# Optimization experiments

Hardware: AMD Instinct MI355X
Metric: run time of the kernel (lower is better)

The kernel has to match this reference:

```python
import jax, jax.numpy as jnp
import numpy as np

H = 12  # num_heads

def _alibi_bias(num_heads, n, dtype):
    # slopes: ratio**i for i in 1..H, ratio = 2**(-8/H)
    ratio = 2.0 ** (-8.0 / num_heads)
    slopes = ratio ** jnp.arange(1, num_heads + 1, dtype=jnp.float32)  # [H]
    pos = jnp.arange(n)
    rel = jnp.abs(pos[None, :] - pos[:, None]).astype(jnp.float32)  # [N,N]
    return (-slopes[:, None, None] * rel[None]).astype(dtype)  # [H,N,N]

def setup_inputs() -> dict:
    key = jax.random.key(0)
    ks = jax.random.split(key, 5)
    B, N, C = 16, 1024, 768
    s = 0.02
    return {
        "x": jax.random.normal(ks[0], (B, N, C), jnp.float32),
        "w_qkv": jax.random.normal(ks[1], (3 * C, C), jnp.float32) * s,
        "b_qkv": jax.random.normal(ks[2], (3 * C,), jnp.float32) * s,
        "w_proj": jax.random.normal(ks[3], (C, C), jnp.float32) * s,
        "b_proj": jax.random.normal(ks[4], (C,), jnp.float32) * s,
    }

def reference(x, w_qkv, b_qkv, w_proj, b_proj):
    B, N, C = x.shape
    D = C // H
    scale = D ** -0.5
    qkv = x @ w_qkv.T + b_qkv                       # [B,N,3C]
    qkv = qkv.reshape(B, N, 3, H, D)
    q = qkv[:, :, 0].transpose(0, 2, 1, 3)          # [B,H,N,D]
    k = qkv[:, :, 1].transpose(0, 2, 1, 3)
    v = qkv[:, :, 2].transpose(0, 2, 1, 3)
    bias = _alibi_bias(H, N, x.dtype)               # [H,N,N]
    scores = jnp.einsum('bhnd,bhmd->bhnm', q, k) * scale + bias[None]
    attn = jax.nn.softmax(scores, axis=-1)
    out = jnp.einsum('bhnm,bhmd->bhnd', attn, v)    # [B,H,N,D]
    out = out.transpose(0, 2, 1, 3).reshape(B, N, C)
    return out @ w_proj.T + b_proj
```

## Files before the change

kernel.cpp:

```cpp
#include <hip/hip_runtime.h>


typedef unsigned short u16;
typedef unsigned int u32;
typedef __attribute__((ext_vector_type(8))) short short8;
typedef __attribute__((ext_vector_type(4))) float f32x4;

__device__ __forceinline__ u16 f2bf(float f) {
    u32 u = __float_as_uint(f);
    u32 r = u + 0x7FFFu + ((u >> 16) & 1u);
    return (u16)(r >> 16);
}

__device__ __forceinline__ f32x4 mfma16(short8 a, short8 b, f32x4 c) {
    return __builtin_amdgcn_mfma_f32_16x16x32_bf16(a, b, c, 0, 0, 0);
}
__device__ __forceinline__ u32 cvtpk_bf16(float lo, float hi) {
    u32 r;
    asm("v_cvt_pk_bf16_f32 %0, %1, %2" : "=v"(r) : "v"(lo), "v"(hi));
    return r;
}

typedef __attribute__((address_space(1))) const unsigned int gu32_t;
typedef __attribute__((address_space(3))) unsigned int su32_t;
__device__ __forceinline__ void gl16(const u16* g, u16* s) {
    __builtin_amdgcn_global_load_lds((gu32_t*)g, (su32_t*)s, 16, 0, 0);
}

__global__ void cvt_f32_bf16(const float* __restrict__ src, u16* __restrict__ dst, int n4) {
    int i = blockIdx.x * blockDim.x + threadIdx.x;
    int stride = gridDim.x * blockDim.x;
    for (int idx = i; idx < n4; idx += stride) {
        float4 v = *(const float4*)(src + (size_t)idx * 4);
        ushort4 o;
        o.x = f2bf(v.x); o.y = f2bf(v.y); o.z = f2bf(v.z); o.w = f2bf(v.w);
        *(ushort4*)(dst + (size_t)idx * 4) = o;
    }
}

template <int EPI>
__global__ __launch_bounds__(256) void gemm_nt(
    const u16* __restrict__ A, const u16* __restrict__ Bw,
    const float* __restrict__ bias, u16* __restrict__ outb, float* __restrict__ outf,
    int nTilesN)
{
    constexpr int K = 768;
    __shared__ __align__(16) u16 lA[2][128 * 32];
    __shared__ __align__(16) u16 lB[2][128 * 32];

    int tid = threadIdx.x;
    int bid = blockIdx.x;
    int nwg = gridDim.x;
    int cpx = nwg >> 3;
    int swz = (bid & 7) * cpx + (bid >> 3);
    int bm = swz / nTilesN;
    int bn = swz - bm * nTilesN;
    int m0 = bm * 128, n0 = bn * 128;

    int sr = tid >> 2;
    int sc = (tid & 3) << 3;
    const u16* pA = A + (size_t)(m0 + sr) * K + sc;
    const u16* pB = Bw + (size_t)(n0 + sr) * K + sc;
    int lo = tid * 8;

    gl16(pA, &lA[0][lo]);
    gl16(pA + (size_t)64 * K, &lA[0][lo + 2048]);
    gl16(pB, &lB[0][lo]);
    gl16(pB + (size_t)64 * K, &lB[0][lo + 2048]);

    int w = tid >> 6, lane = tid & 63;
    int wr = (w >> 1) << 6, wc = (w & 1) << 6;
    int fq = lane >> 4, fr = lane & 15;
    f32x4 acc[4][4] = {};

    constexpr int nkt = K / 32;

    for (int kt = 0; kt < nkt; ++kt) {
        int cur = kt & 1;
        __syncthreads();
        if (kt + 1 < nkt) {
            int nxt = cur ^ 1;
            const u16* qA = pA + (kt + 1) * 32;
            const u16* qB = pB + (kt + 1) * 32;
            gl16(qA, &lA[nxt][lo]);
            gl16(qA + (size_t)64 * K, &lA[nxt][lo + 2048]);
            gl16(qB, &lB[nxt][lo]);
            gl16(qB + (size_t)64 * K, &lB[nxt][lo + 2048]);
        }
        short8 af[4], bfr[4];
#pragma unroll
        for (int i = 0; i < 4; ++i)
            af[i] = *(const short8*)&lA[cur][(wr + i * 16 + fr) * 32 + fq * 8];
#pragma unroll
        for (int j = 0; j < 4; ++j)
            bfr[j] = *(const short8*)&lB[cur][(wc + j * 16 + fr) * 32 + fq * 8];
        __builtin_amdgcn_s_setprio(1);
#pragma unroll
        for (int i = 0; i < 4; ++i)
#pragma unroll
            for (int j = 0; j < 4; ++j)
                acc[i][j] = mfma16(af[i], bfr[j], acc[i][j]);
        __builtin_amdgcn_s_setprio(0);
    }

    if (EPI == 0) {
        int nbase = n0 + wc;
        int s = nbase / 768;
        int hh = (nbase % 768) >> 6;
        int b = m0 >> 10;
        int i0 = (m0 & 1023) + wr;
        u16* obase = outb + (((size_t)s * 16 + b) * 12 + hh) * 1024 * 64;
#pragma unroll
        for (int j = 0; j < 4; ++j) {
            float bval = bias[nbase + j * 16 + fr];
            int d = j * 16 + fr;
#pragma unroll
            for (int i = 0; i < 4; ++i) {
                int r0 = i0 + i * 16 + fq * 4;
#pragma unroll
                for (int r = 0; r < 4; ++r)
                    obase[(size_t)(r0 + r) * 64 + d] = f2bf(acc[i][j][r] + bval);
            }
        }
    } else {
#pragma unroll
        for (int j = 0; j < 4; ++j) {
            int col = n0 + wc + j * 16 + fr;
            float bval = bias[col];
#pragma unroll
            for (int i = 0; i < 4; ++i) {
                int row0 = m0 + wr + i * 16 + fq * 4;
#pragma unroll
                for (int r = 0; r < 4; ++r)
                    outf[(size_t)(row0 + r) * 768 + col] = acc[i][j][r] + bval;
            }
        }
    }
}

__global__ __launch_bounds__(256) void attn_alibi(
    const u16* __restrict__ QKV, u16* __restrict__ att)
{
    int g = blockIdx.x;
    int xcd = g & 7;
    int idx = g >> 3;
    int qt = idx & 15;
    int bh = xcd * 24 + (idx >> 4);
    int h = bh % 12;
    int b = bh / 12;
    int q0 = qt * 64;
    const u16* Qg = QKV + (size_t)bh * 65536;
    const u16* Kg = QKV + (size_t)(192 + bh) * 65536;
    const u16* Vg = QKV + (size_t)(384 + bh) * 65536;

    __shared__ __align__(16) u16 Qs[64][72];
    __shared__ __align__(16) u16 Ks[64][72];
    __shared__ __align__(16) u16 Vt[64][72];
    __shared__ __align__(16) u16 Ps[64][72];

    int tid = threadIdx.x, w = tid >> 6, lane = tid & 63;
    int fq = lane >> 4, fr = lane & 15;

    for (int c = tid; c < 512; c += 256) {
        int r = c >> 3, d = (c & 7) * 8;
        *(uint4*)&Qs[r][d] = *(const uint4*)(Qg + (size_t)(q0 + r) * 64 + d);
    }
    __syncthreads();
    short8 aq0 = *(const short8*)&Qs[w * 16 + fr][fq * 8];
    short8 aq1 = *(const short8*)&Qs[w * 16 + fr][32 + fq * 8];

    const float C1 = 0.125f * 1.44269504f;
    float c2 = __builtin_amdgcn_exp2f(-(2.0f / 3.0f) * (float)(h + 1)) * 1.44269504f;
    int distThr = (int)(40.0f / c2);
    int lo_kv = q0 - 63 - distThr;
    int hi_kv = q0 + 63 + distThr;
    int t_lo = (lo_kv <= 0) ? 0 : (lo_kv >> 6);
    int t_hi = (hi_kv >= 1023) ? 15 : (hi_kv >> 6);

    int sr0 = tid >> 3;
    int sr1 = sr0 + 32;
    int sc = (tid & 7) * 8;
    int vswz = (tid & 7) << 3;

    uint4 kr0 = *(const uint4*)(Kg + (size_t)(t_lo * 64 + sr0) * 64 + sc);
    uint4 kr1 = *(const uint4*)(Kg + (size_t)(t_lo * 64 + sr1) * 64 + sc);
    uint4 vr0 = *(const uint4*)(Vg + (size_t)(t_lo * 64 + sr0) * 64 + sc);
    uint4 vr1 = *(const uint4*)(Vg + (size_t)(t_lo * 64 + sr1) * 64 + sc);

    float di = (float)(q0 + w * 16 + fr - fq * 4);
    float lsum = 0.f;
    f32x4 acc[4] = {};

    for (int it = t_lo; it <= t_hi; ++it) {
        __syncthreads();
        *(uint4*)&Ks[sr0][sc] = kr0;
        *(uint4*)&Ks[sr1][sc] = kr1;
        {
            const u16* v0 = (const u16*)&vr0;
            const u16* v1 = (const u16*)&vr1;
#pragma unroll
            for (int jj = 0; jj < 8; ++jj) {
                Vt[sc + jj][sr0 ^ vswz] = v0[jj];
                Vt[sc + jj][sr1 ^ vswz] = v1[jj];
            }
        }
        __syncthreads();

        if (it < t_hi) {
            int kvn = (it + 1) * 64;
            kr0 = *(const uint4*)(Kg + (size_t)(kvn + sr0) * 64 + sc);
            kr1 = *(const uint4*)(Kg + (size_t)(kvn + sr1) * 64 + sc);
            vr0 = *(const uint4*)(Vg + (size_t)(kvn + sr0) * 64 + sc);
            vr1 = *(const uint4*)(Vg + (size_t)(kvn + sr1) * 64 + sc);
        }

        f32x4 sfr[4];
        __builtin_amdgcn_s_setprio(1);
#pragma unroll
        for (int ct = 0; ct < 4; ++ct) {
            short8 bk0 = *(const short8*)&Ks[ct * 16 + fr][fq * 8];
            short8 bk1 = *(const short8*)&Ks[ct * 16 + fr][32 + fq * 8];
            f32x4 s0 = {0.f, 0.f, 0.f, 0.f};
            s0 = mfma16(bk0, aq0, s0);
            s0 = mfma16(bk1, aq1, s0);
            sfr[ct] = s0;
        }
        __builtin_amdgcn_s_setprio(0);

        float dkv = di - (float)(it * 64);
#pragma unroll
        for (int ct = 0; ct < 4; ++ct) {
#pragma unroll
            for (int rp = 0; rp < 2; ++rp) {
                float t0 = dkv - (float)(ct * 16 + rp * 2);
                float e0 = __builtin_amdgcn_exp2f(fmaf(sfr[ct][rp * 2], C1, -c2 * fabsf(t0)));
                float e1 = __builtin_amdgcn_exp2f(fmaf(sfr[ct][rp * 2 + 1], C1, -c2 * fabsf(t0 - 1.0f)));
                lsum += e0 + e1;
                *(u32*)&Ps[w * 16 + fr][ct * 16 + fq * 4 + rp * 2] = cvtpk_bf16(e0, e1);
            }
        }

        short8 pa0 = *(const short8*)&Ps[w * 16 + fr][fq * 8];
        short8 pa1 = *(const short8*)&Ps[w * 16 + fr][32 + fq * 8];
        __builtin_amdgcn_s_setprio(1);
#pragma unroll
        for (int dt = 0; dt < 4; ++dt) {
            int row = dt * 16 + fr;
            int swzr = (row >> 3) << 3;
            short8 bv0 = *(const short8*)&Vt[row][(fq * 8) ^ swzr];
            short8 bv1 = *(const short8*)&Vt[row][(32 + fq * 8) ^ swzr];
            acc[dt] = mfma16(pa0, bv0, acc[dt]);
            acc[dt] = mfma16(pa1, bv1, acc[dt]);
        }
        __builtin_amdgcn_s_setprio(0);
    }

    float l = lsum;
    l += __shfl_xor(l, 16);
    l += __shfl_xor(l, 32);
    float rlo = 1.0f / l;
    float rl[4];
#pragma unroll
    for (int r = 0; r < 4; ++r)
        rl[r] = __shfl(rlo, fq * 4 + r);

#pragma unroll
    for (int dt = 0; dt < 4; ++dt)
#pragma unroll
        for (int r = 0; r < 4; ++r) {
            int ig = q0 + w * 16 + fq * 4 + r;
            att[((size_t)(b * 1024 + ig) * 12 + h) * 64 + dt * 16 + fr] =
                (u16)cvtpk_bf16(acc[dt][r] * rl[r], 0.f);
        }
}

extern "C" void kernel_launch(void* const* d_in, const int* in_sizes, int n_in,
                              void* d_out, int out_size, void* d_ws, size_t ws_size,
                              hipStream_t stream) {
    const float* x      = (const float*)d_in[0];
    const float* w_qkv  = (const float*)d_in[1];
    const float* b_qkv  = (const float*)d_in[2];
    const float* w_proj = (const float*)d_in[3];
    const float* b_proj = (const float*)d_in[4];
    float* out = (float*)d_out;

    char* ws = (char*)d_ws;
    u16* Xb     = (u16*)ws;
    u16* Wqkvb  = (u16*)(ws + 25165824);
    u16* Wprojb = (u16*)(ws + 28704768);
    u16* QKVb   = (u16*)(ws + 29884416);
    u16* Attb   = Xb;

    cvt_f32_bf16<<<2048, 256, 0, stream>>>(x, Xb, 12582912 / 4);
    cvt_f32_bf16<<<1728, 256, 0, stream>>>(w_qkv, Wqkvb, 1769472 / 4);
    cvt_f32_bf16<<<576, 256, 0, stream>>>(w_proj, Wprojb, 589824 / 4);

    gemm_nt<0><<<128 * 18, 256, 0, stream>>>(Xb, Wqkvb, b_qkv, QKVb, nullptr, 18);
    attn_alibi<<<3072, 256, 0, stream>>>(QKVb, Attb);
    gemm_nt<1><<<128 * 6, 256, 0, stream>>>(Attb, Wprojb, b_proj, nullptr, out, 6);
}
```

Before: 210.8 us.

## Triple-buffer GEMM LDS pipeline and fuse conversion kernels into one launch

The GEMM now keeps three LDS stages and prefetches two k-tiles ahead. It waits on vmcnt explicitly, so one raw barrier per iteration replaces __syncthreads and loads stay in flight longer. The three fp32-to-bf16 conversion launches become a single kernel that walks all three tensors, removing two launches. The extra LDS stage raises shared memory per block to 48KB, which may cut occupancy, and the vmcnt counts assume exactly four global_load_lds ops per stage.

```diff
diff --git a/kernel.cpp b/kernel.cpp
--- a/kernel.cpp
+++ b/kernel.cpp
@@ -27,14 +27,22 @@
     __builtin_amdgcn_global_load_lds((gu32_t*)g, (su32_t*)s, 16, 0, 0);
 }
 
-__global__ void cvt_f32_bf16(const float* __restrict__ src, u16* __restrict__ dst, int n4) {
+__global__ void cvt_all(const float* __restrict__ x, const float* __restrict__ wq,
+                        const float* __restrict__ wp, u16* __restrict__ Xb,
+                        u16* __restrict__ Wqkvb, u16* __restrict__ Wprojb) {
     int i = blockIdx.x * blockDim.x + threadIdx.x;
     int stride = gridDim.x * blockDim.x;
-    for (int idx = i; idx < n4; idx += stride) {
-        float4 v = *(const float4*)(src + (size_t)idx * 4);
+    for (int idx = i; idx < 3735552; idx += stride) {
+        const float* src;
+        u16* dst;
+        int k;
+        if (idx < 3145728) { src = x; dst = Xb; k = idx; }
+        else if (idx < 3588096) { src = wq; dst = Wqkvb; k = idx - 3145728; }
+        else { src = wp; dst = Wprojb; k = idx - 3588096; }
+        float4 v = *(const float4*)(src + (size_t)k * 4);
         ushort4 o;
         o.x = f2bf(v.x); o.y = f2bf(v.y); o.z = f2bf(v.z); o.w = f2bf(v.w);
-        *(ushort4*)(dst + (size_t)idx * 4) = o;
+        *(ushort4*)(dst + (size_t)k * 4) = o;
     }
 }
 
@@ -45,8 +53,9 @@
     int nTilesN)
 {
     constexpr int K = 768;
-    __shared__ __align__(16) u16 lA[2][128 * 32];
-    __shared__ __align__(16) u16 lB[2][128 * 32];
+    constexpr int nkt = K / 32;
+    __shared__ __align__(16) u16 lA[3][128 * 32];
+    __shared__ __align__(16) u16 lB[3][128 * 32];
 
     int tid = threadIdx.x;
     int bid = blockIdx.x;
@@ -67,25 +76,31 @@
     gl16(pA + (size_t)64 * K, &lA[0][lo + 2048]);
     gl16(pB, &lB[0][lo]);
     gl16(pB + (size_t)64 * K, &lB[0][lo + 2048]);
+    gl16(pA + 32, &lA[1][lo]);
+    gl16(pA + (size_t)64 * K + 32, &lA[1][lo + 2048]);
+    gl16(pB + 32, &lB[1][lo]);
+    gl16(pB + (size_t)64 * K + 32, &lB[1][lo + 2048]);
 
     int w = tid >> 6, lane = tid & 63;
     int wr = (w >> 1) << 6, wc = (w & 1) << 6;
     int fq = lane >> 4, fr = lane & 15;
     f32x4 acc[4][4] = {};
 
-    constexpr int nkt = K / 32;
-
     for (int kt = 0; kt < nkt; ++kt) {
-        int cur = kt & 1;
-        __syncthreads();
-        if (kt + 1 < nkt) {
-            int nxt = cur ^ 1;
-            const u16* qA = pA + (kt + 1) * 32;
-            const u16* qB = pB + (kt + 1) * 32;
-            gl16(qA, &lA[nxt][lo]);
-            gl16(qA + (size_t)64 * K, &lA[nxt][lo + 2048]);
-            gl16(qB, &lB[nxt][lo]);
-            gl16(qB + (size_t)64 * K, &lB[nxt][lo + 2048]);
+        int cur = kt % 3;
+        if (kt < nkt - 1) { asm volatile("s_waitcnt vmcnt(4)" ::: "memory"); }
+        else              { asm volatile("s_waitcnt vmcnt(0)" ::: "memory"); }
+        __builtin_amdgcn_sched_barrier(0);
+        __builtin_amdgcn_s_barrier();
+        __builtin_amdgcn_sched_barrier(0);
+        if (kt + 2 < nkt) {
+            int nx = (kt + 2) % 3;
+            const u16* qA = pA + (kt + 2) * 32;
+            const u16* qB = pB + (kt + 2) * 32;
+            gl16(qA, &lA[nx][lo]);
+            gl16(qA + (size_t)64 * K, &lA[nx][lo + 2048]);
+            gl16(qB, &lB[nx][lo]);
+            gl16(qB + (size_t)64 * K, &lB[nx][lo + 2048]);
         }
         short8 af[4], bfr[4];
 #pragma unroll
@@ -291,9 +306,7 @@
     u16* QKVb   = (u16*)(ws + 29884416);
     u16* Attb   = Xb;
 
-    cvt_f32_bf16<<<2048, 256, 0, stream>>>(x, Xb, 12582912 / 4);
-    cvt_f32_bf16<<<1728, 256, 0, stream>>>(w_qkv, Wqkvb, 1769472 / 4);
-    cvt_f32_bf16<<<576, 256, 0, stream>>>(w_proj, Wprojb, 589824 / 4);
+    cvt_all<<<2048, 256, 0, stream>>>(x, w_qkv, w_proj, Xb, Wqkvb, Wprojb);
 
     gemm_nt<0><<<128 * 18, 256, 0, stream>>>(Xb, Wqkvb, b_qkv, QKVb, nullptr, 18);
     attn_alibi<<<3072, 256, 0, stream>>>(QKVb, Attb);
```

Result: faster. 204.2 us (-3.1%).
